# Kernel optimization log

Measured on AMD Instinct MI355X. Metric: run time of the kernel, lower is better.

Reference implementation:

```python
import jax, jax.numpy as jnp
import numpy as np

B, DIM = 32, 4096
NQ, NKV, HD = 32, 8, 128
NREP = NQ // NKV
MAX_SEQ = 2048
START_POS = 2048  # decode position; cache prefix of length START_POS is attended


def setup_inputs() -> dict:
    key = jax.random.key(0)
    ks = jax.random.split(key, 10)
    s = 0.02
    return {
        "x": jax.random.normal(ks[0], (B, 1, DIM), jnp.float32),
        "start_pos": START_POS,
        "freqs_real": jax.random.normal(ks[1], (1, HD // 2), jnp.float32),
        "freqs_imag": jax.random.normal(ks[2], (1, HD // 2), jnp.float32),
        "wq": jax.random.normal(ks[3], (DIM, NQ * HD), jnp.float32) * s,
        "wk": jax.random.normal(ks[4], (DIM, NKV * HD), jnp.float32) * s,
        "wv": jax.random.normal(ks[5], (DIM, NKV * HD), jnp.float32) * s,
        "wo": jax.random.normal(ks[6], (NQ * HD, DIM), jnp.float32) * s,
        "cache_k": jax.random.normal(ks[7], (B, MAX_SEQ, NKV, HD), jnp.float32),
        "cache_v": jax.random.normal(ks[8], (B, MAX_SEQ, NKV, HD), jnp.float32),
    }


def _rope(t, fr, fi):
    # t: [b, s, h, hd]; rotate pairs (even, odd) by complex freqs [s, hd/2]
    tf = t.astype(jnp.float32)
    b, s, h, hd = tf.shape
    tr = tf.reshape(b, s, h, hd // 2, 2)
    x0, x1 = tr[..., 0], tr[..., 1]
    frb = fr.reshape(1, s, 1, hd // 2)
    fib = fi.reshape(1, s, 1, hd // 2)
    o0 = x0 * frb - x1 * fib
    o1 = x0 * fib + x1 * frb
    return jnp.stack([o0, o1], axis=-1).reshape(b, s, h, hd).astype(t.dtype)


def reference(x, start_pos, freqs_real, freqs_imag, wq, wk, wv, wo, cache_k, cache_v):
    b, s, _ = x.shape  # s == 1 (decode step)
    xq = (x @ wq).reshape(b, s, NQ, HD)
    xk = (x @ wk).reshape(b, s, NKV, HD)
    xv = (x @ wv).reshape(b, s, NKV, HD)
    xq = _rope(xq, freqs_real, freqs_imag)
    xk = _rope(xk, freqs_real, freqs_imag)

    # KV-cache write at position start_pos-1, then read prefix [:start_pos]
    cache_k = jax.lax.dynamic_update_slice(cache_k, xk, (0, start_pos - 1, 0, 0))
    cache_v = jax.lax.dynamic_update_slice(cache_v, xv, (0, start_pos - 1, 0, 0))
    keys = cache_k[:, :start_pos]    # [b, L, NKV, HD]
    values = cache_v[:, :start_pos]

    # grouped-query attention (equivalent to repeat_kv, kv-major head order)
    qg = xq.reshape(b, s, NKV, NREP, HD)
    scores = jnp.einsum('bigrd,bjgd->bgrij', qg, keys) / jnp.sqrt(jnp.float32(HD))
    attn = jax.nn.softmax(scores.astype(jnp.float32), axis=-1).astype(xq.dtype)
    out = jnp.einsum('bgrij,bjgd->bgrid', attn, values)  # [b, NKV, NREP, s, HD]
    out = out.reshape(b, NQ, s, HD).transpose(0, 2, 1, 3).reshape(b, s, NQ * HD)
    return out @ wo
```

## Files before the change

kernel.cpp:

```cpp
#include <hip/hip_runtime.h>

#define DIMX 4096
#define NB   32
#define NQH  32
#define NKVH 8
#define HDIM 128
#define SEQ  2048
#define NCHUNK 32
#define CHUNK  64

__global__ __launch_bounds__(256) void k_qkv(const float* __restrict__ x,
                                             const float* __restrict__ wq,
                                             const float* __restrict__ wk,
                                             const float* __restrict__ wv,
                                             float* __restrict__ partial) {
  __shared__ float xs[32][132];
  const int t = threadIdx.x;
  const int d0 = blockIdx.y * 128;
  for (int e = t; e < 32 * 32; e += 256) {
    const int b = e >> 5, q = e & 31;
    *reinterpret_cast<float4*>(&xs[b][q * 4]) =
        *reinterpret_cast<const float4*>(&x[b * DIMX + d0 + q * 4]);
  }
  __syncthreads();
  const int base = blockIdx.x * 512;
  const float* W; int ncols, lbase;
  if (base < 4096)      { W = wq; ncols = 4096; lbase = base; }
  else if (base < 5120) { W = wk; ncols = 1024; lbase = base - 4096; }
  else                  { W = wv; ncols = 1024; lbase = base - 5120; }
  const float* WA = W + (size_t)d0 * ncols + lbase + t;
  const float* WB = WA + 256;
  float accA[32], accB[32];
  #pragma unroll
  for (int b = 0; b < 32; ++b) { accA[b] = 0.f; accB[b] = 0.f; }
  for (int dd = 0; dd < 128; dd += 4) {
    const float a0 = WA[(size_t)(dd + 0) * ncols];
    const float a1 = WA[(size_t)(dd + 1) * ncols];
    const float a2 = WA[(size_t)(dd + 2) * ncols];
    const float a3 = WA[(size_t)(dd + 3) * ncols];
    const float b0 = WB[(size_t)(dd + 0) * ncols];
    const float b1 = WB[(size_t)(dd + 1) * ncols];
    const float b2 = WB[(size_t)(dd + 2) * ncols];
    const float b3 = WB[(size_t)(dd + 3) * ncols];
    #pragma unroll
    for (int b = 0; b < 32; ++b) {
      const float4 xv = *reinterpret_cast<const float4*>(&xs[b][dd]);
      accA[b] += xv.x * a0 + xv.y * a1 + xv.z * a2 + xv.w * a3;
      accB[b] += xv.x * b0 + xv.y * b1 + xv.z * b2 + xv.w * b3;
    }
  }
  #pragma unroll
  for (int b = 0; b < 32; ++b) {
    partial[((size_t)blockIdx.y * 32 + b) * 6144 + base + t]       = accA[b];
    partial[((size_t)blockIdx.y * 32 + b) * 6144 + base + 256 + t] = accB[b];
  }
}

__global__ __launch_bounds__(256) void k_combine_rope(const float* __restrict__ partial,
                                                      const float* __restrict__ fr,
                                                      const float* __restrict__ fi,
                                                      float* __restrict__ qkv) {
  const int p = blockIdx.x * 256 + threadIdx.x;
  const int b = p / 1536, cq = p % 1536;
  const int col = cq * 4;
  float sx = 0.f, sy = 0.f, sz = 0.f, sw = 0.f;
  for (int c = 0; c < 32; ++c) {
    const float4 v = *reinterpret_cast<const float4*>(&partial[((size_t)c * 32 + b) * 6144 + col]);
    sx += v.x; sy += v.y; sz += v.z; sw += v.w;
  }
  if (col < 5120) {
    const int i = (col & 127) >> 1;
    const float cr0 = fr[i],     ci0 = fi[i];
    const float cr1 = fr[i + 1], ci1 = fi[i + 1];
    const float o0 = sx * cr0 - sy * ci0;
    const float o1 = sx * ci0 + sy * cr0;
    const float o2 = sz * cr1 - sw * ci1;
    const float o3 = sz * ci1 + sw * cr1;
    sx = o0; sy = o1; sz = o2; sw = o3;
  }
  *reinterpret_cast<float4*>(&qkv[(size_t)b * 6144 + col]) = make_float4(sx, sy, sz, sw);
}

__global__ __launch_bounds__(256) void k_attn(const float* __restrict__ qkv,
                                              const float* __restrict__ cache_k,
                                              const float* __restrict__ cache_v,
                                              float* __restrict__ opart,
                                              float* __restrict__ ml) {
  __shared__ float qs[4 * 128];
  __shared__ float ks[CHUNK * 132];
  const int bx = blockIdx.x;
  const int c = bx & 31, g = (bx >> 5) & 7, b = bx >> 8;
  const int t = threadIdx.x;

  if (t < 128) {
    *reinterpret_cast<float4*>(&qs[t * 4]) =
        *reinterpret_cast<const float4*>(&qkv[(size_t)b * 6144 + g * 512 + t * 4]);
  }
  const int j0 = c * CHUNK;
  for (int e = t; e < CHUNK * 32; e += 256) {
    const int j = e >> 5, q4i = e & 31;
    const int jg = j0 + j;
    const float* ksrc = (jg == 2047) ? &qkv[(size_t)b * 6144 + 4096 + g * 128]
                                     : &cache_k[(((size_t)b * SEQ + jg) * NKVH + g) * HDIM];
    *reinterpret_cast<float4*>(&ks[j * 132 + q4i * 4]) =
        *reinterpret_cast<const float4*>(&ksrc[q4i * 4]);
  }
  __syncthreads();

  const int rep = t >> 6, lane = t & 63;
  float s = 0.f;
  const float4* ksr = reinterpret_cast<const float4*>(&ks[lane * 132]);
  const float4* qsr = reinterpret_cast<const float4*>(&qs[rep * 128]);
  #pragma unroll
  for (int dq = 0; dq < 32; ++dq) {
    const float4 k4 = ksr[dq];
    const float4 q4 = qsr[dq];
    s += k4.x * q4.x + k4.y * q4.y + k4.z * q4.z + k4.w * q4.w;
  }
  s *= 0.08838834764831845f;

  float m = s;
  #pragma unroll
  for (int o = 32; o > 0; o >>= 1) m = fmaxf(m, __shfl_xor(m, o));
  const float p = __expf(s - m);
  float l = p;
  #pragma unroll
  for (int o = 32; o > 0; o >>= 1) l += __shfl_xor(l, o);

  float a0 = 0.f, a1 = 0.f;
  const float* vrow0 = &cache_v[(((size_t)b * SEQ + j0) * NKVH + g) * HDIM];
  const float* vlast = &qkv[(size_t)b * 6144 + 5120 + g * 128];
  #pragma unroll 8
  for (int jj = 0; jj < CHUNK; ++jj) {
    const float pp = __shfl(p, jj);
    const float* vsrc = (j0 + jj == 2047) ? vlast : (vrow0 + (size_t)jj * NKVH * HDIM);
    const float2 v2 = *reinterpret_cast<const float2*>(&vsrc[lane * 2]);
    a0 += pp * v2.x;
    a1 += pp * v2.y;
  }
  const int bgr = (b * 8 + g) * 4 + rep;
  *reinterpret_cast<float2*>(&opart[((size_t)bgr * NCHUNK + c) * 128 + lane * 2]) =
      make_float2(a0, a1);
  if (lane == 0) {
    ml[((size_t)bgr * NCHUNK + c) * 2]     = m;
    ml[((size_t)bgr * NCHUNK + c) * 2 + 1] = l;
  }
}

__global__ __launch_bounds__(128) void k_attn_combine(const float* __restrict__ opart,
                                                      const float* __restrict__ ml,
                                                      float* __restrict__ attn_out) {
  const int bgr = blockIdx.x;
  const int d = threadIdx.x;
  float M = -1e30f;
  for (int c = 0; c < NCHUNK; ++c) M = fmaxf(M, ml[((size_t)bgr * NCHUNK + c) * 2]);
  float L = 0.f, acc = 0.f;
  for (int c = 0; c < NCHUNK; ++c) {
    const float w = __expf(ml[((size_t)bgr * NCHUNK + c) * 2] - M);
    L += ml[((size_t)bgr * NCHUNK + c) * 2 + 1] * w;
    acc += opart[((size_t)bgr * NCHUNK + c) * 128 + d] * w;
  }
  attn_out[(size_t)bgr * 128 + d] = acc / L;
}

__global__ __launch_bounds__(256) void k_oproj(const float* __restrict__ attn_out,
                                               const float* __restrict__ wo,
                                               float* __restrict__ partial) {
  __shared__ float xs[32][132];
  const int t = threadIdx.x;
  const int d0 = blockIdx.y * 128;
  for (int e = t; e < 32 * 32; e += 256) {
    const int b = e >> 5, q = e & 31;
    *reinterpret_cast<float4*>(&xs[b][q * 4]) =
        *reinterpret_cast<const float4*>(&attn_out[b * DIMX + d0 + q * 4]);
  }
  __syncthreads();
  const int base = blockIdx.x * 512;
  const float* WA = wo + (size_t)d0 * 4096 + base + t;
  const float* WB = WA + 256;
  float accA[32], accB[32];
  #pragma unroll
  for (int b = 0; b < 32; ++b) { accA[b] = 0.f; accB[b] = 0.f; }
  for (int dd = 0; dd < 128; dd += 4) {
    const float a0 = WA[(size_t)(dd + 0) * 4096];
    const float a1 = WA[(size_t)(dd + 1) * 4096];
    const float a2 = WA[(size_t)(dd + 2) * 4096];
    const float a3 = WA[(size_t)(dd + 3) * 4096];
    const float b0 = WB[(size_t)(dd + 0) * 4096];
    const float b1 = WB[(size_t)(dd + 1) * 4096];
    const float b2 = WB[(size_t)(dd + 2) * 4096];
    const float b3 = WB[(size_t)(dd + 3) * 4096];
    #pragma unroll
    for (int b = 0; b < 32; ++b) {
      const float4 xv = *reinterpret_cast<const float4*>(&xs[b][dd]);
      accA[b] += xv.x * a0 + xv.y * a1 + xv.z * a2 + xv.w * a3;
      accB[b] += xv.x * b0 + xv.y * b1 + xv.z * b2 + xv.w * b3;
    }
  }
  #pragma unroll
  for (int b = 0; b < 32; ++b) {
    partial[((size_t)blockIdx.y * 32 + b) * 4096 + base + t]       = accA[b];
    partial[((size_t)blockIdx.y * 32 + b) * 4096 + base + 256 + t] = accB[b];
  }
}

__global__ __launch_bounds__(256) void k_final(const float* __restrict__ partial,
                                               float* __restrict__ out) {
  const int e = blockIdx.x * 256 + threadIdx.x;
  const int b = e >> 12, col = e & 4095;
  float s = 0.f;
  for (int c = 0; c < 32; ++c) s += partial[((size_t)c * 32 + b) * 4096 + col];
  out[e] = s;
}

extern "C" void kernel_launch(void* const* d_in, const int* in_sizes, int n_in,
                              void* d_out, int out_size, void* d_ws, size_t ws_size,
                              hipStream_t stream) {
  const float* x  = (const float*)d_in[0];
  const float* fr = (const float*)d_in[2];
  const float* fi = (const float*)d_in[3];
  const float* wq = (const float*)d_in[4];
  const float* wk = (const float*)d_in[5];
  const float* wv = (const float*)d_in[6];
  const float* wo = (const float*)d_in[7];
  const float* ck = (const float*)d_in[8];
  const float* cv = (const float*)d_in[9];
  float* out = (float*)d_out;

  float* ws = (float*)d_ws;
  float* big  = ws;
  float* qkv  = ws + 6291456;
  float* mlb  = ws + 6488064;
  float* attn = ws + 6553600;

  k_qkv<<<dim3(12, 32), 256, 0, stream>>>(x, wq, wk, wv, big);
  k_combine_rope<<<192, 256, 0, stream>>>(big, fr, fi, qkv);
  k_attn<<<32 * 8 * NCHUNK, 256, 0, stream>>>(qkv, ck, cv, big, mlb);
  k_attn_combine<<<1024, 128, 0, stream>>>(big, mlb, attn);
  k_oproj<<<dim3(8, 32), 256, 0, stream>>>(attn, wo, big);
  k_final<<<512, 256, 0, stream>>>(big, out);
}
```

Before: 274.7 us.

## Restructure attention kernel so each thread handles all four query heads per KV group

The attention kernel now launches one 512-thread block per (batch, chunk) covering all 8 KV groups. Each wave handles one group, and each lane reads its own key row directly from global memory and computes scores for all four query heads of the group. The score computation no longer goes through a shared-memory K tile. Each V row is loaded once and applied to four probability values, where before it was reread per head; this cuts redundant K/V global reads. The trade-offs are per-lane strided float4 key loads (less coalesced), higher register pressure, and fewer, larger blocks.

New measurement: 272.0 us. Within noise of the previous version (-1.0%).

```diff
diff --git a/kernel.cpp b/kernel.cpp
--- a/kernel.cpp
+++ b/kernel.cpp
@@ -81,69 +81,97 @@
   *reinterpret_cast<float4*>(&qkv[(size_t)b * 6144 + col]) = make_float4(sx, sy, sz, sw);
 }
 
-__global__ __launch_bounds__(256) void k_attn(const float* __restrict__ qkv,
+__global__ __launch_bounds__(512) void k_attn(const float* __restrict__ qkv,
                                               const float* __restrict__ cache_k,
                                               const float* __restrict__ cache_v,
                                               float* __restrict__ opart,
                                               float* __restrict__ ml) {
-  __shared__ float qs[4 * 128];
-  __shared__ float ks[CHUNK * 132];
+  __shared__ float qls[4096];
+  __shared__ float ps[8 * 64 * 4];
   const int bx = blockIdx.x;
-  const int c = bx & 31, g = (bx >> 5) & 7, b = bx >> 8;
+  const int c = bx & 31, b = bx >> 5;
   const int t = threadIdx.x;
-
-  if (t < 128) {
-    *reinterpret_cast<float4*>(&qs[t * 4]) =
-        *reinterpret_cast<const float4*>(&qkv[(size_t)b * 6144 + g * 512 + t * 4]);
-  }
+  const int g = t >> 6, lane = t & 63;
+
+  {
+    const float4* src = reinterpret_cast<const float4*>(&qkv[(size_t)b * 6144]);
+    float4* dst = reinterpret_cast<float4*>(qls);
+    for (int e = t; e < 1024; e += 512) dst[e] = src[e];
+  }
+  __syncthreads();
+
   const int j0 = c * CHUNK;
-  for (int e = t; e < CHUNK * 32; e += 256) {
-    const int j = e >> 5, q4i = e & 31;
-    const int jg = j0 + j;
-    const float* ksrc = (jg == 2047) ? &qkv[(size_t)b * 6144 + 4096 + g * 128]
-                                     : &cache_k[(((size_t)b * SEQ + jg) * NKVH + g) * HDIM];
-    *reinterpret_cast<float4*>(&ks[j * 132 + q4i * 4]) =
-        *reinterpret_cast<const float4*>(&ksrc[q4i * 4]);
-  }
-  __syncthreads();
-
-  const int rep = t >> 6, lane = t & 63;
-  float s = 0.f;
-  const float4* ksr = reinterpret_cast<const float4*>(&ks[lane * 132]);
-  const float4* qsr = reinterpret_cast<const float4*>(&qs[rep * 128]);
-  #pragma unroll
+  const int jg = j0 + lane;
+  const float* krow = (jg == 2047) ? &qkv[(size_t)b * 6144 + 4096 + g * 128]
+                                   : &cache_k[(((size_t)b * SEQ + jg) * NKVH + g) * HDIM];
+  const float4* krow4 = reinterpret_cast<const float4*>(krow);
+  const float4* q4g = reinterpret_cast<const float4*>(&qls[g * 512]);
+  float s0 = 0.f, s1 = 0.f, s2 = 0.f, s3 = 0.f;
+  #pragma unroll 8
   for (int dq = 0; dq < 32; ++dq) {
-    const float4 k4 = ksr[dq];
-    const float4 q4 = qsr[dq];
-    s += k4.x * q4.x + k4.y * q4.y + k4.z * q4.z + k4.w * q4.w;
-  }
-  s *= 0.08838834764831845f;
-
-  float m = s;
-  #pragma unroll
-  for (int o = 32; o > 0; o >>= 1) m = fmaxf(m, __shfl_xor(m, o));
-  const float p = __expf(s - m);
-  float l = p;
-  #pragma unroll
-  for (int o = 32; o > 0; o >>= 1) l += __shfl_xor(l, o);
-
-  float a0 = 0.f, a1 = 0.f;
-  const float* vrow0 = &cache_v[(((size_t)b * SEQ + j0) * NKVH + g) * HDIM];
+    const float4 k4 = krow4[dq];
+    const float4 qa = q4g[dq];
+    const float4 qb = q4g[32 + dq];
+    const float4 qc = q4g[64 + dq];
+    const float4 qd = q4g[96 + dq];
+    s0 += k4.x * qa.x + k4.y * qa.y + k4.z * qa.z + k4.w * qa.w;
+    s1 += k4.x * qb.x + k4.y * qb.y + k4.z * qb.z + k4.w * qb.w;
+    s2 += k4.x * qc.x + k4.y * qc.y + k4.z * qc.z + k4.w * qc.w;
+    s3 += k4.x * qd.x + k4.y * qd.y + k4.z * qd.z + k4.w * qd.w;
+  }
+  const float sc = 0.08838834764831845f;
+  s0 *= sc; s1 *= sc; s2 *= sc; s3 *= sc;
+
+  float m0 = s0, m1 = s1, m2 = s2, m3 = s3;
+  #pragma unroll
+  for (int o = 32; o > 0; o >>= 1) {
+    m0 = fmaxf(m0, __shfl_xor(m0, o));
+    m1 = fmaxf(m1, __shfl_xor(m1, o));
+    m2 = fmaxf(m2, __shfl_xor(m2, o));
+    m3 = fmaxf(m3, __shfl_xor(m3, o));
+  }
+  float p0 = __expf(s0 - m0), p1 = __expf(s1 - m1);
+  float p2 = __expf(s2 - m2), p3 = __expf(s3 - m3);
+  float l0 = p0, l1 = p1, l2 = p2, l3 = p3;
+  #pragma unroll
+  for (int o = 32; o > 0; o >>= 1) {
+    l0 += __shfl_xor(l0, o);
+    l1 += __shfl_xor(l1, o);
+    l2 += __shfl_xor(l2, o);
+    l3 += __shfl_xor(l3, o);
+  }
+  reinterpret_cast<float4*>(ps)[g * 64 + lane] = make_float4(p0, p1, p2, p3);
+  __syncthreads();
+
+  float a00 = 0.f, a01 = 0.f, a10 = 0.f, a11 = 0.f;
+  float a20 = 0.f, a21 = 0.f, a30 = 0.f, a31 = 0.f;
+  const float4* psg = reinterpret_cast<const float4*>(ps) + g * 64;
+  const float* vbase = &cache_v[(((size_t)b * SEQ + j0) * NKVH + g) * HDIM];
   const float* vlast = &qkv[(size_t)b * 6144 + 5120 + g * 128];
   #pragma unroll 8
   for (int jj = 0; jj < CHUNK; ++jj) {
-    const float pp = __shfl(p, jj);
-    const float* vsrc = (j0 + jj == 2047) ? vlast : (vrow0 + (size_t)jj * NKVH * HDIM);
-    const float2 v2 = *reinterpret_cast<const float2*>(&vsrc[lane * 2]);
-    a0 += pp * v2.x;
-    a1 += pp * v2.y;
-  }
-  const int bgr = (b * 8 + g) * 4 + rep;
-  *reinterpret_cast<float2*>(&opart[((size_t)bgr * NCHUNK + c) * 128 + lane * 2]) =
-      make_float2(a0, a1);
+    const float4 p4 = psg[jj];
+    const float* vr = (j0 + jj == 2047) ? vlast : (vbase + (size_t)jj * (NKVH * HDIM));
+    const float2 v2 = *reinterpret_cast<const float2*>(&vr[lane * 2]);
+    a00 += p4.x * v2.x; a01 += p4.x * v2.y;
+    a10 += p4.y * v2.x; a11 += p4.y * v2.y;
+    a20 += p4.z * v2.x; a21 += p4.z * v2.y;
+    a30 += p4.w * v2.x; a31 += p4.w * v2.y;
+  }
+  const int bg = b * NKVH + g;
+  *reinterpret_cast<float2*>(&opart[(((size_t)(bg * 4 + 0)) * NCHUNK + c) * 128 + lane * 2]) = make_float2(a00, a01);
+  *reinterpret_cast<float2*>(&opart[(((size_t)(bg * 4 + 1)) * NCHUNK + c) * 128 + lane * 2]) = make_float2(a10, a11);
+  *reinterpret_cast<float2*>(&opart[(((size_t)(bg * 4 + 2)) * NCHUNK + c) * 128 + lane * 2]) = make_float2(a20, a21);
+  *reinterpret_cast<float2*>(&opart[(((size_t)(bg * 4 + 3)) * NCHUNK + c) * 128 + lane * 2]) = make_float2(a30, a31);
   if (lane == 0) {
-    ml[((size_t)bgr * NCHUNK + c) * 2]     = m;
-    ml[((size_t)bgr * NCHUNK + c) * 2 + 1] = l;
+    ml[(((size_t)(bg * 4 + 0)) * NCHUNK + c) * 2]     = m0;
+    ml[(((size_t)(bg * 4 + 0)) * NCHUNK + c) * 2 + 1] = l0;
+    ml[(((size_t)(bg * 4 + 1)) * NCHUNK + c) * 2]     = m1;
+    ml[(((size_t)(bg * 4 + 1)) * NCHUNK + c) * 2 + 1] = l1;
+    ml[(((size_t)(bg * 4 + 2)) * NCHUNK + c) * 2]     = m2;
+    ml[(((size_t)(bg * 4 + 2)) * NCHUNK + c) * 2 + 1] = l2;
+    ml[(((size_t)(bg * 4 + 3)) * NCHUNK + c) * 2]     = m3;
+    ml[(((size_t)(bg * 4 + 3)) * NCHUNK + c) * 2 + 1] = l3;
   }
 }
 
@@ -235,7 +263,7 @@
 
   k_qkv<<<dim3(12, 32), 256, 0, stream>>>(x, wq, wk, wv, big);
   k_combine_rope<<<192, 256, 0, stream>>>(big, fr, fi, qkv);
-  k_attn<<<32 * 8 * NCHUNK, 256, 0, stream>>>(qkv, ck, cv, big, mlb);
+  k_attn<<<32 * NCHUNK, 512, 0, stream>>>(qkv, ck, cv, big, mlb);
   k_attn_combine<<<1024, 128, 0, stream>>>(big, mlb, attn);
   k_oproj<<<dim3(8, 32), 256, 0, stream>>>(attn, wo, big);
   k_final<<<512, 256, 0, stream>>>(big, out);
```
